# Performance work log

Measured on AMD Instinct MI355X. Metric: run time of the kernel, lower is better.

## Reference

```python
import jax, jax.numpy as jnp
import numpy as np

N_NODES = 100000
N_EDGES = 1600000
F_IN = 64
HEADS = 2
D_HEAD = 64  # hidden_channels per head
F_OUT = HEADS * D_HEAD  # 128 (concat=True)
NEG_SLOPE = 0.2


def setup_inputs() -> dict:
    key = jax.random.key(0)
    ks = jax.random.split(key, 10)
    x = jax.random.normal(ks[0], (N_NODES, F_IN), dtype=jnp.float32)
    edge_index = jax.random.randint(ks[1], (2, N_EDGES), 0, N_NODES, dtype=jnp.int32)
    perm = jax.random.permutation(ks[2], N_NODES).astype(jnp.int32)
    s = 0.05
    W_src = jax.random.normal(ks[3], (F_IN, F_OUT), dtype=jnp.float32) * s
    W_dst = jax.random.normal(ks[4], (F_IN, F_OUT), dtype=jnp.float32) * s
    a_src = jax.random.normal(ks[5], (HEADS, D_HEAD), dtype=jnp.float32) * s
    a_dst = jax.random.normal(ks[6], (HEADS, D_HEAD), dtype=jnp.float32) * s
    bias = jnp.zeros((F_OUT,), dtype=jnp.float32)
    prelu_w = jnp.full((F_OUT,), 0.25, dtype=jnp.float32)  # torch PReLU default init
    return {"x": x, "edge_index": edge_index, "perm": perm,
            "W_src": W_src, "W_dst": W_dst, "a_src": a_src, "a_dst": a_dst,
            "bias": bias, "prelu_w": prelu_w}


def _gat_prelu(x, edge_index, W_src, W_dst, a_src, a_dst, bias, prelu_w):
    # PyG GATConv, add_self_loops=False, heads=HEADS, concat=True, then PReLU.
    N = x.shape[0]
    src, dst = edge_index[0], edge_index[1]
    xs = (x @ W_src).reshape(N, HEADS, D_HEAD)  # source-side projection
    xd = (x @ W_dst).reshape(N, HEADS, D_HEAD)  # destination-side projection
    al_s = jnp.einsum('nhd,hd->nh', xs, a_src)  # [N,H]
    al_d = jnp.einsum('nhd,hd->nh', xd, a_dst)  # [N,H]
    e = jax.nn.leaky_relu(al_s[src] + al_d[dst], NEG_SLOPE)  # [E,H]
    # softmax over incoming edges of each destination node
    m = jax.ops.segment_max(e, dst, num_segments=N)  # [N,H]
    ex = jnp.exp(e - m[dst])
    den = jax.ops.segment_sum(ex, dst, num_segments=N)  # [N,H]
    alpha = ex / (den[dst] + 1e-16)  # [E,H]
    msg = xs[src] * alpha[:, :, None]  # [E,H,D]
    out = jax.ops.segment_sum(msg, dst, num_segments=N)  # [N,H,D]
    out = out.reshape(N, F_OUT) + bias
    return jnp.where(out >= 0, out, prelu_w * out)


def reference(x, edge_index, perm, W_src, W_dst, a_src, a_dst, bias, prelu_w):
    # DGI forward: positive embedding, corrupted (negative) embedding, summary
    pos_z = _gat_prelu(x, edge_index, W_src, W_dst, a_src, a_dst, bias, prelu_w)
    x_cor = x[perm]  # corruption: permute node features, keep edges
    neg_z = _gat_prelu(x_cor, edge_index, W_src, W_dst, a_src, a_dst, bias, prelu_w)
    summary = jax.nn.sigmoid(pos_z.mean(axis=0))
    return pos_z, neg_z, summary
```

## Files before the change

### kernel.cpp

```cpp
#include <hip/hip_runtime.h>
#include <hip/hip_bf16.h>

#define F_IN   64
#define HEADS  2
#define D_HEAD 64
#define F_OUT  128
#define NEG_SLOPE 0.2f

#define AGG_GRID 2048
#define CAP 48

__global__ __launch_bounds__(256, 2) void proj_kernel(
    const float* __restrict__ x, const float* __restrict__ W,
    const float* __restrict__ Wd,
    const float* __restrict__ as_, const float* __restrict__ ad_,
    __hip_bfloat16* __restrict__ xsb, float* __restrict__ als, float* __restrict__ ald,
    int* __restrict__ cnt, int N)
{
    __shared__ float xsh[8][64];
    __shared__ float a2dsh[128];
    int t = threadIdx.x;
    int c    = t & 127;
    int slot = t >> 7;
    int h    = c >> 6;
    int j    = c & 63;

    for (int g = blockIdx.x * 256 + t; g < N + 128; g += gridDim.x * 256) cnt[g] = 0;

    float Wcol[64];
    #pragma unroll
    for (int k = 0; k < 64; ++k) Wcol[k] = W[k * 128 + c];

    if (t < 128) {
        int jj = t >> 1, hh = t & 1;
        float sd = 0.f;
        #pragma unroll 8
        for (int d = 0; d < 64; ++d) sd += Wd[jj * 128 + hh * 64 + d] * ad_[hh * 64 + d];
        a2dsh[t] = sd;
    }

    float asv = as_[h * 64 + j];

    for (long long base = (long long)blockIdx.x * 8; base < N; base += (long long)gridDim.x * 8) {
        __syncthreads();
        {
            int r  = t >> 5;
            int kk = (t & 31) * 2;
            long long nn = base + r;
            float2 v = (nn < N) ? *reinterpret_cast<const float2*>(x + nn * 64 + kk)
                                : make_float2(0.f, 0.f);
            xsh[r][kk]     = v.x;
            xsh[r][kk + 1] = v.y;
        }
        __syncthreads();

        float acc0 = 0.f, acc1 = 0.f, acc2 = 0.f, acc3 = 0.f;
        #pragma unroll
        for (int k4 = 0; k4 < 64; k4 += 4) {
            float4 x0 = *reinterpret_cast<const float4*>(&xsh[slot    ][k4]);
            float4 x1 = *reinterpret_cast<const float4*>(&xsh[slot + 2][k4]);
            float4 x2 = *reinterpret_cast<const float4*>(&xsh[slot + 4][k4]);
            float4 x3 = *reinterpret_cast<const float4*>(&xsh[slot + 6][k4]);
            acc0 += x0.x * Wcol[k4] + x0.y * Wcol[k4+1] + x0.z * Wcol[k4+2] + x0.w * Wcol[k4+3];
            acc1 += x1.x * Wcol[k4] + x1.y * Wcol[k4+1] + x1.z * Wcol[k4+2] + x1.w * Wcol[k4+3];
            acc2 += x2.x * Wcol[k4] + x2.y * Wcol[k4+1] + x2.z * Wcol[k4+2] + x2.w * Wcol[k4+3];
            acc3 += x3.x * Wcol[k4] + x3.y * Wcol[k4+1] + x3.z * Wcol[k4+2] + x3.w * Wcol[k4+3];
        }

        float a2dv = a2dsh[j * 2 + h];
        float rs0 = acc0 * asv, rd0 = xsh[slot    ][j] * a2dv;
        float rs1 = acc1 * asv, rd1 = xsh[slot + 2][j] * a2dv;
        float rs2 = acc2 * asv, rd2 = xsh[slot + 4][j] * a2dv;
        float rs3 = acc3 * asv, rd3 = xsh[slot + 6][j] * a2dv;
        #pragma unroll
        for (int off = 32; off; off >>= 1) {
            rs0 += __shfl_down(rs0, off, 64); rd0 += __shfl_down(rd0, off, 64);
            rs1 += __shfl_down(rs1, off, 64); rd1 += __shfl_down(rd1, off, 64);
            rs2 += __shfl_down(rs2, off, 64); rd2 += __shfl_down(rd2, off, 64);
            rs3 += __shfl_down(rs3, off, 64); rd3 += __shfl_down(rd3, off, 64);
        }

        long long n0 = base + slot;
        if (n0     < N) xsb[(n0    ) * 128 + c] = __float2bfloat16(acc0);
        if (n0 + 2 < N) xsb[(n0 + 2) * 128 + c] = __float2bfloat16(acc1);
        if (n0 + 4 < N) xsb[(n0 + 4) * 128 + c] = __float2bfloat16(acc2);
        if (n0 + 6 < N) xsb[(n0 + 6) * 128 + c] = __float2bfloat16(acc3);
        if (j == 0) {
            if (n0     < N) { als[(n0    ) * 2 + h] = rs0; ald[(n0    ) * 2 + h] = rd0; }
            if (n0 + 2 < N) { als[(n0 + 2) * 2 + h] = rs1; ald[(n0 + 2) * 2 + h] = rd1; }
            if (n0 + 4 < N) { als[(n0 + 4) * 2 + h] = rs2; ald[(n0 + 4) * 2 + h] = rd2; }
            if (n0 + 6 < N) { als[(n0 + 6) * 2 + h] = rs3; ald[(n0 + 6) * 2 + h] = rd3; }
        }
    }
}

__global__ void scatter_kernel(const int2* __restrict__ src2, const int2* __restrict__ dst2,
                               const int* __restrict__ perm,
                               int* __restrict__ cnt, int2* __restrict__ csr2, int E2) {
    int i = blockIdx.x * blockDim.x + threadIdx.x;
    if (i >= E2) return;
    int2 s = src2[i];
    int2 d = dst2[i];
    int slot0 = atomicAdd(&cnt[d.x], 1);
    if (slot0 < CAP) csr2[d.x * CAP + slot0] = make_int2(s.x, perm[s.x]);
    int slot1 = atomicAdd(&cnt[d.y], 1);
    if (slot1 < CAP) csr2[d.y * CAP + slot1] = make_int2(s.y, perm[s.y]);
}

__global__ __launch_bounds__(256) void aggfused_kernel(
    const int* __restrict__ cnt,
    const int2* __restrict__ csr2,
    const int* __restrict__ perm,
    const float* __restrict__ als, const float* __restrict__ ald,
    const unsigned* __restrict__ xsu,
    const float* __restrict__ bias, const float* __restrict__ pw,
    float* __restrict__ zP, float* __restrict__ zN,
    float* __restrict__ colsum, int N)
{
    int t    = threadIdx.x;
    int wid  = t >> 6;
    int lane = t & 63;
    int col  = lane * 2;
    int h    = lane >> 5;
    int rel  = lane & 31;
    float bi0 = bias[col], bi1 = bias[col + 1];
    float pw0 = pw[col],   pw1 = pw[col + 1];
    float sum0 = 0.f, sum1 = 0.f;

    for (int n = blockIdx.x * 4 + wid; n < N; n += AGG_GRID * 4) {
        int e0 = n * CAP;
        int e1 = e0 + min(cnt[n], CAP);
        float aldvP = ald[n * 2 + h];
        float aldvN = ald[perm[n] * 2 + h];
        float denP = 0.f, aP0 = 0.f, aP1 = 0.f;
        float denN = 0.f, aN0 = 0.f, aN1 = 0.f;

        for (int cb = e0; cb < e1; cb += 32) {
            int idx = cb + rel;
            bool valid = idx < e1;
            int idxc = valid ? idx : e0;
            int2 sp2 = csr2[idxc];
            int spP = sp2.x;
            int spN = sp2.y;
            float scP = als[spP * 2 + h] + aldvP;
            float scN = als[spN * 2 + h] + aldvN;
            scP = (scP >= 0.f) ? scP : NEG_SLOPE * scP;
            scN = (scN >= 0.f) ? scN : NEG_SLOPE * scN;
            float wP = valid ? __expf(fminf(scP, 60.f)) : 0.f;
            float wN = valid ? __expf(fminf(scN, 60.f)) : 0.f;
            denP += wP;
            denN += wN;

            int ec = min(32, e1 - cb);
            int hb = h << 5;
            for (int i = 0; i < ec; i += 8) {
                float wp_[8], wn_[8]; int pp_[8], pn_[8]; unsigned vp_[8], vn_[8];
                #pragma unroll
                for (int k = 0; k < 8; ++k) {
                    wp_[k] = __shfl(wP, hb + i + k, 64);
                    pp_[k] = __shfl(spP, i + k, 64);
                    wn_[k] = __shfl(wN, hb + i + k, 64);
                    pn_[k] = __shfl(spN, i + k, 64);
                }
                #pragma unroll
                for (int k = 0; k < 8; ++k) {
                    vp_[k] = xsu[pp_[k] * 64 + lane];
                    vn_[k] = xsu[pn_[k] * 64 + lane];
                }
                #pragma unroll
                for (int k = 0; k < 8; ++k) {
                    float fp0 = __uint_as_float((vp_[k] & 0xffffu) << 16);
                    float fp1 = __uint_as_float(vp_[k] & 0xffff0000u);
                    aP0 += wp_[k] * fp0;
                    aP1 += wp_[k] * fp1;
                    float fn0 = __uint_as_float((vn_[k] & 0xffffu) << 16);
                    float fn1 = __uint_as_float(vn_[k] & 0xffff0000u);
                    aN0 += wn_[k] * fn0;
                    aN1 += wn_[k] * fn1;
                }
            }
        }

        #pragma unroll
        for (int off = 16; off; off >>= 1) {
            denP += __shfl_xor(denP, off, 64);
            denN += __shfl_xor(denN, off, 64);
        }

        float inv = 1.f / (denP + 1e-16f);
        float v0 = aP0 * inv + bi0;
        float v1 = aP1 * inv + bi1;
        v0 = (v0 >= 0.f) ? v0 : pw0 * v0;
        v1 = (v1 >= 0.f) ? v1 : pw1 * v1;
        *reinterpret_cast<float2*>(zP + (long long)n * 128 + col) = make_float2(v0, v1);
        sum0 += v0; sum1 += v1;

        inv = 1.f / (denN + 1e-16f);
        v0 = aN0 * inv + bi0;
        v1 = aN1 * inv + bi1;
        v0 = (v0 >= 0.f) ? v0 : pw0 * v0;
        v1 = (v1 >= 0.f) ? v1 : pw1 * v1;
        *reinterpret_cast<float2*>(zN + (long long)n * 128 + col) = make_float2(v0, v1);
    }

    __shared__ float sh[512];
    sh[t * 2]     = sum0;
    sh[t * 2 + 1] = sum1;
    __syncthreads();
    if (wid == 0) {
        float s0 = sh[t * 2]     + sh[(t + 64) * 2]     + sh[(t + 128) * 2]     + sh[(t + 192) * 2];
        float s1 = sh[t * 2 + 1] + sh[(t + 64) * 2 + 1] + sh[(t + 128) * 2 + 1] + sh[(t + 192) * 2 + 1];
        atomicAdd(&colsum[col],     s0);
        atomicAdd(&colsum[col + 1], s1);
    }
}

__global__ void summary_kernel(const float* __restrict__ colsum, float* __restrict__ out,
                               float invN)
{
    int c = threadIdx.x;
    float m = colsum[c] * invN;
    out[c] = 1.f / (1.f + expf(-m));
}

extern "C" void kernel_launch(void* const* d_in, const int* in_sizes, int n_in,
                              void* d_out, int out_size, void* d_ws, size_t ws_size,
                              hipStream_t stream) {
    const float* x      = (const float*)d_in[0];
    const int*   ei     = (const int*)  d_in[1];
    const int*   perm   = (const int*)  d_in[2];
    const float* Wsrc   = (const float*)d_in[3];
    const float* Wdst   = (const float*)d_in[4];
    const float* a_src  = (const float*)d_in[5];
    const float* a_dst  = (const float*)d_in[6];
    const float* bias   = (const float*)d_in[7];
    const float* prelu  = (const float*)d_in[8];

    const int N = in_sizes[0] / F_IN;
    const int E = in_sizes[1] / 2;
    const int* src = ei;
    const int* dst = ei + E;

    float* ws = (float*)d_ws;
    long long off = 0;
    float* als    = ws + off; off += 2LL * N;
    float* ald    = ws + off; off += 2LL * N;
    int*   cnt    = (int*)(ws + off); off += N;
    float* colsum = ws + off; off += 128;
    int2*  csr2   = (int2*)(ws + off); off += 2LL * N * CAP;
    unsigned* xsu = (unsigned*)(ws + off); off += (long long)N * 64;

    float* outP = (float*)d_out;
    float* outN = outP + (long long)N * F_OUT;
    float* outS = outN + (long long)N * F_OUT;

    proj_kernel<<<1024, 256, 0, stream>>>(x, Wsrc, Wdst, a_src, a_dst,
                                          (__hip_bfloat16*)xsu, als, ald, cnt, N);

    const int E2 = E / 2;
    const int eb2 = (E2 + 255) / 256;
    scatter_kernel<<<eb2, 256, 0, stream>>>((const int2*)src, (const int2*)dst, perm,
                                            cnt, csr2, E2);

    aggfused_kernel<<<AGG_GRID, 256, 0, stream>>>(cnt, csr2, perm, als, ald, xsu,
                                                  bias, prelu, outP, outN, colsum, N);

    summary_kernel<<<1, 128, 0, stream>>>(colsum, outS, 1.0f / (float)N);
}
```

Before: 359.1 us.

## Process two destination nodes per wave with prefetched metadata and nontemporal IO

The aggregation kernel now has each wavefront handle a pair of destination nodes at once, interleaving their gather bursts so that more independent memory loads are in flight. Counts and destination attention logits for the next pair are loaded one iteration early, hiding their latency. CSR reads and output stores use nontemporal hints so that streaming data is less likely to evict cached feature rows. The cost is higher register pressure, which may reduce occupancy, and extra control flow when the two nodes have different degrees.

```diff
diff --git a/kernel.cpp b/kernel.cpp
--- a/kernel.cpp
+++ b/kernel.cpp
@@ -9,6 +9,9 @@
 
 #define AGG_GRID 2048
 #define CAP 48
+
+__device__ __forceinline__ float bf_lo(unsigned v) { return __uint_as_float((v & 0xffffu) << 16); }
+__device__ __forceinline__ float bf_hi(unsigned v) { return __uint_as_float(v & 0xffff0000u); }
 
 __global__ __launch_bounds__(256, 2) void proj_kernel(
     const float* __restrict__ x, const float* __restrict__ W,
@@ -107,6 +110,30 @@
     if (slot1 < CAP) csr2[d.y * CAP + slot1] = make_int2(s.y, perm[s.y]);
 }
 
+#define BURST(spP, spN, wP, wN, i, accP0, accP1, accN0, accN1)                     \
+    do {                                                                           \
+        float wp_[8], wn_[8]; int pp_[8], pn_[8]; unsigned vp_[8], vn_[8];         \
+        _Pragma("unroll")                                                          \
+        for (int k = 0; k < 8; ++k) {                                              \
+            wp_[k] = __shfl(wP, hb + (i) + k, 64);                                 \
+            pp_[k] = __shfl(spP, (i) + k, 64);                                     \
+            wn_[k] = __shfl(wN, hb + (i) + k, 64);                                 \
+            pn_[k] = __shfl(spN, (i) + k, 64);                                     \
+        }                                                                          \
+        _Pragma("unroll")                                                          \
+        for (int k = 0; k < 8; ++k) {                                              \
+            vp_[k] = xsu[pp_[k] * 64 + lane];                                      \
+            vn_[k] = xsu[pn_[k] * 64 + lane];                                      \
+        }                                                                          \
+        _Pragma("unroll")                                                          \
+        for (int k = 0; k < 8; ++k) {                                              \
+            accP0 += wp_[k] * bf_lo(vp_[k]);                                       \
+            accP1 += wp_[k] * bf_hi(vp_[k]);                                       \
+            accN0 += wn_[k] * bf_lo(vn_[k]);                                       \
+            accN1 += wn_[k] * bf_hi(vn_[k]);                                       \
+        }                                                                          \
+    } while (0)
+
 __global__ __launch_bounds__(256) void aggfused_kernel(
     const int* __restrict__ cnt,
     const int2* __restrict__ csr2,
@@ -117,90 +144,148 @@
     float* __restrict__ zP, float* __restrict__ zN,
     float* __restrict__ colsum, int N)
 {
+    const int STEP = AGG_GRID * 4;
     int t    = threadIdx.x;
     int wid  = t >> 6;
     int lane = t & 63;
     int col  = lane * 2;
     int h    = lane >> 5;
     int rel  = lane & 31;
+    int hb   = h << 5;
     float bi0 = bias[col], bi1 = bias[col + 1];
     float pw0 = pw[col],   pw1 = pw[col + 1];
     float sum0 = 0.f, sum1 = 0.f;
 
-    for (int n = blockIdx.x * 4 + wid; n < N; n += AGG_GRID * 4) {
-        int e0 = n * CAP;
-        int e1 = e0 + min(cnt[n], CAP);
-        float aldvP = ald[n * 2 + h];
-        float aldvN = ald[perm[n] * 2 + h];
-        float denP = 0.f, aP0 = 0.f, aP1 = 0.f;
-        float denN = 0.f, aN0 = 0.f, aN1 = 0.f;
-
-        for (int cb = e0; cb < e1; cb += 32) {
-            int idx = cb + rel;
-            bool valid = idx < e1;
-            int idxc = valid ? idx : e0;
-            int2 sp2 = csr2[idxc];
-            int spP = sp2.x;
-            int spN = sp2.y;
-            float scP = als[spP * 2 + h] + aldvP;
-            float scN = als[spN * 2 + h] + aldvN;
-            scP = (scP >= 0.f) ? scP : NEG_SLOPE * scP;
-            scN = (scN >= 0.f) ? scN : NEG_SLOPE * scN;
-            float wP = valid ? __expf(fminf(scP, 60.f)) : 0.f;
-            float wN = valid ? __expf(fminf(scN, 60.f)) : 0.f;
-            denP += wP;
-            denN += wN;
-
-            int ec = min(32, e1 - cb);
-            int hb = h << 5;
-            for (int i = 0; i < ec; i += 8) {
-                float wp_[8], wn_[8]; int pp_[8], pn_[8]; unsigned vp_[8], vn_[8];
-                #pragma unroll
-                for (int k = 0; k < 8; ++k) {
-                    wp_[k] = __shfl(wP, hb + i + k, 64);
-                    pp_[k] = __shfl(spP, i + k, 64);
-                    wn_[k] = __shfl(wN, hb + i + k, 64);
-                    pn_[k] = __shfl(spN, i + k, 64);
-                }
-                #pragma unroll
-                for (int k = 0; k < 8; ++k) {
-                    vp_[k] = xsu[pp_[k] * 64 + lane];
-                    vn_[k] = xsu[pn_[k] * 64 + lane];
-                }
-                #pragma unroll
-                for (int k = 0; k < 8; ++k) {
-                    float fp0 = __uint_as_float((vp_[k] & 0xffffu) << 16);
-                    float fp1 = __uint_as_float(vp_[k] & 0xffff0000u);
-                    aP0 += wp_[k] * fp0;
-                    aP1 += wp_[k] * fp1;
-                    float fn0 = __uint_as_float((vn_[k] & 0xffffu) << 16);
-                    float fn1 = __uint_as_float(vn_[k] & 0xffff0000u);
-                    aN0 += wn_[k] * fn0;
-                    aN1 += wn_[k] * fn1;
-                }
+    const int NP = (N + 1) >> 1;
+    int g0 = blockIdx.x * 4 + wid;
+
+    int cA_c = 0, cB_c = 0;
+    float aPA_c = 0.f, aNA_c = 0.f, aPB_c = 0.f, aNB_c = 0.f;
+    if (g0 < NP) {
+        int nA = g0 * 2, nB = nA + 1;
+        cA_c = min(cnt[nA], CAP);
+        aPA_c = ald[nA * 2 + h];
+        aNA_c = ald[perm[nA] * 2 + h];
+        if (nB < N) {
+            cB_c = min(cnt[nB], CAP);
+            aPB_c = ald[nB * 2 + h];
+            aNB_c = ald[perm[nB] * 2 + h];
+        }
+    }
+
+    for (int g = g0; g < NP; g += STEP) {
+        int g2 = g + STEP;
+        int cA_n = 0, cB_n = 0;
+        float aPA_n = 0.f, aNA_n = 0.f, aPB_n = 0.f, aNB_n = 0.f;
+        if (g2 < NP) {
+            int nA2 = g2 * 2, nB2 = nA2 + 1;
+            cA_n = min(cnt[nA2], CAP);
+            aPA_n = ald[nA2 * 2 + h];
+            aNA_n = ald[perm[nA2] * 2 + h];
+            if (nB2 < N) {
+                cB_n = min(cnt[nB2], CAP);
+                aPB_n = ald[nB2 * 2 + h];
+                aNB_n = ald[perm[nB2] * 2 + h];
+            }
+        }
+
+        int nA = g * 2, nB = nA + 1;
+        int cA = cA_c, cB = cB_c;
+        long long eA = (long long)nA * CAP, eB = (long long)nB * CAP;
+
+        float denPA = 0.f, aPA0 = 0.f, aPA1 = 0.f, denNA = 0.f, aNA0 = 0.f, aNA1 = 0.f;
+        float denPB = 0.f, aPB0 = 0.f, aPB1 = 0.f, denNB = 0.f, aNB0 = 0.f, aNB1 = 0.f;
+
+        float wPA = 0.f, wNA = 0.f, wPB = 0.f, wNB = 0.f;
+        int spPA = 0, spNA = 0, spPB = 0, spNB = 0;
+
+        int cmax = max(cA, cB);
+        for (int rbase = 0; rbase < cmax; rbase += 32) {
+            if (rbase < cA) {
+                int o = rbase + rel;
+                bool v = o < cA;
+                long long raw = __builtin_nontemporal_load(
+                    (const long long*)(csr2 + (v ? eA + o : eA)));
+                spPA = v ? (int)(unsigned)(raw & 0xffffffffLL) : 0;
+                spNA = v ? (int)(raw >> 32) : 0;
+                float scP = als[spPA * 2 + h] + aPA_c;
+                float scN = als[spNA * 2 + h] + aNA_c;
+                scP = (scP >= 0.f) ? scP : NEG_SLOPE * scP;
+                scN = (scN >= 0.f) ? scN : NEG_SLOPE * scN;
+                wPA = v ? __expf(fminf(scP, 60.f)) : 0.f;
+                wNA = v ? __expf(fminf(scN, 60.f)) : 0.f;
+                denPA += wPA; denNA += wNA;
+            }
+            if (rbase < cB) {
+                int o = rbase + rel;
+                bool v = o < cB;
+                long long raw = __builtin_nontemporal_load(
+                    (const long long*)(csr2 + (v ? eB + o : eB)));
+                spPB = v ? (int)(unsigned)(raw & 0xffffffffLL) : 0;
+                spNB = v ? (int)(raw >> 32) : 0;
+                float scP = als[spPB * 2 + h] + aPB_c;
+                float scN = als[spNB * 2 + h] + aNB_c;
+                scP = (scP >= 0.f) ? scP : NEG_SLOPE * scP;
+                scN = (scN >= 0.f) ? scN : NEG_SLOPE * scN;
+                wPB = v ? __expf(fminf(scP, 60.f)) : 0.f;
+                wNB = v ? __expf(fminf(scN, 60.f)) : 0.f;
+                denPB += wPB; denNB += wNB;
+            }
+
+            int ecA = min(32, cA - rbase);
+            int ecB = min(32, cB - rbase);
+            for (int i = 0; i < 32; i += 8) {
+                if (i < ecA) BURST(spPA, spNA, wPA, wNA, i, aPA0, aPA1, aNA0, aNA1);
+                if (i < ecB) BURST(spPB, spNB, wPB, wNB, i, aPB0, aPB1, aNB0, aNB1);
+                if (i + 8 >= ecA && i + 8 >= ecB) break;
             }
         }
 
         #pragma unroll
         for (int off = 16; off; off >>= 1) {
-            denP += __shfl_xor(denP, off, 64);
-            denN += __shfl_xor(denN, off, 64);
-        }
-
-        float inv = 1.f / (denP + 1e-16f);
-        float v0 = aP0 * inv + bi0;
-        float v1 = aP1 * inv + bi1;
-        v0 = (v0 >= 0.f) ? v0 : pw0 * v0;
-        v1 = (v1 >= 0.f) ? v1 : pw1 * v1;
-        *reinterpret_cast<float2*>(zP + (long long)n * 128 + col) = make_float2(v0, v1);
-        sum0 += v0; sum1 += v1;
-
-        inv = 1.f / (denN + 1e-16f);
-        v0 = aN0 * inv + bi0;
-        v1 = aN1 * inv + bi1;
-        v0 = (v0 >= 0.f) ? v0 : pw0 * v0;
-        v1 = (v1 >= 0.f) ? v1 : pw1 * v1;
-        *reinterpret_cast<float2*>(zN + (long long)n * 128 + col) = make_float2(v0, v1);
+            denPA += __shfl_xor(denPA, off, 64);
+            denNA += __shfl_xor(denNA, off, 64);
+            denPB += __shfl_xor(denPB, off, 64);
+            denNB += __shfl_xor(denNB, off, 64);
+        }
+
+        {
+            float inv = 1.f / (denPA + 1e-16f);
+            float v0 = aPA0 * inv + bi0, v1 = aPA1 * inv + bi1;
+            v0 = (v0 >= 0.f) ? v0 : pw0 * v0;
+            v1 = (v1 >= 0.f) ? v1 : pw1 * v1;
+            float2 v2 = make_float2(v0, v1);
+            __builtin_nontemporal_store(*(const double*)&v2,
+                                        (double*)(zP + (long long)nA * 128 + col));
+            sum0 += v0; sum1 += v1;
+            inv = 1.f / (denNA + 1e-16f);
+            v0 = aNA0 * inv + bi0; v1 = aNA1 * inv + bi1;
+            v0 = (v0 >= 0.f) ? v0 : pw0 * v0;
+            v1 = (v1 >= 0.f) ? v1 : pw1 * v1;
+            v2 = make_float2(v0, v1);
+            __builtin_nontemporal_store(*(const double*)&v2,
+                                        (double*)(zN + (long long)nA * 128 + col));
+        }
+        if (nB < N) {
+            float inv = 1.f / (denPB + 1e-16f);
+            float v0 = aPB0 * inv + bi0, v1 = aPB1 * inv + bi1;
+            v0 = (v0 >= 0.f) ? v0 : pw0 * v0;
+            v1 = (v1 >= 0.f) ? v1 : pw1 * v1;
+            float2 v2 = make_float2(v0, v1);
+            __builtin_nontemporal_store(*(const double*)&v2,
+                                        (double*)(zP + (long long)nB * 128 + col));
+            sum0 += v0; sum1 += v1;
+            inv = 1.f / (denNB + 1e-16f);
+            v0 = aNB0 * inv + bi0; v1 = aNB1 * inv + bi1;
+            v0 = (v0 >= 0.f) ? v0 : pw0 * v0;
+            v1 = (v1 >= 0.f) ? v1 : pw1 * v1;
+            v2 = make_float2(v0, v1);
+            __builtin_nontemporal_store(*(const double*)&v2,
+                                        (double*)(zN + (long long)nB * 128 + col));
+        }
+
+        cA_c = cA_n; cB_c = cB_n;
+        aPA_c = aPA_n; aNA_c = aNA_n; aPB_c = aPB_n; aNB_c = aNB_n;
     }
 
     __shared__ float sh[512];
```

Measured after the change: 358.5 us. About the same (-0.1%).
